# Performance work log

Measured on AMD Instinct MI355X. Metric: run time of the kernel, lower is better.

The kernel has to match this reference:

```python
import jax, jax.numpy as jnp
import numpy as np

B, L, D = 4, 512, 1024
E, TOP_K = 16, 4
F = 4 * D  # expert hidden width


def setup_inputs() -> dict:
    key = jax.random.key(0)
    ks = jax.random.split(key, 6)
    scale = 0.02
    return {
        "x": jax.random.normal(ks[0], (B, L, D), jnp.float32),
        "keys": jax.random.normal(ks[1], (E, D), jnp.float32),          # expert_keys
        "w1": jax.random.normal(ks[2], (E, F, D), jnp.float32) * scale,  # Linear(D,4D).weight per expert
        "b1": jnp.zeros((E, F), jnp.float32),
        "w2": jax.random.normal(ks[3], (E, D, F), jnp.float32) * scale,  # Linear(4D,D).weight per expert
        "b2": jnp.zeros((E, D), jnp.float32),
        "rw": jax.random.normal(ks[4], (E, D), jnp.float32) * scale,     # router Linear(D,E).weight
        "rb": jnp.zeros((E,), jnp.float32),
    }


def reference(x, keys, w1, b1, w2, b2, rw, rb):
    # Laplace gate: squared Euclidean distance token-to-expert-key (broadcasted, as in torch)
    diff = x[:, :, None, :] - keys                      # (B,L,E,D)
    dist2 = jnp.sum(diff * diff, axis=-1)               # (B,L,E)
    logits = -dist2 + jnp.einsum('bld,ed->ble', x, rw) + rb

    topv, topi = jax.lax.top_k(logits, TOP_K)           # (B,L,K)
    w = jax.nn.softmax(topv, axis=-1)                   # (B,L,K)

    # Dense all-expert MLP (exact GELU, matching torch nn.GELU default)
    hidden = jax.nn.gelu(jnp.einsum('bld,efd->blef', x, w1) + b1, approximate=False)  # (B,L,E,F)
    exp_out = jnp.einsum('blef,edf->bled', hidden, w2) + b2                            # (B,L,E,D)

    # Gather top-k expert outputs and combine with softmax weights
    sel = jnp.take_along_axis(exp_out, topi[..., None], axis=2)  # (B,L,K,D)
    fused = jnp.sum(w[..., None] * sel, axis=2)                  # (B,L,D)
    return fused
```

## Files before the change

### kernel.cpp

```cpp
#include <hip/hip_runtime.h>

#define B_ 4
#define L_ 512
#define D_ 1024
#define E_ 16
#define K_ 4
#define F_ 4096
#define NTOK (B_*L_)
#define NPAIR (NTOK*K_)

typedef float f32x4 __attribute__((ext_vector_type(4)));
typedef __bf16 bf16x8 __attribute__((ext_vector_type(8)));

__device__ inline unsigned int pack2(float a, float b) {
    unsigned short ua = __builtin_bit_cast(unsigned short, (__bf16)a);
    unsigned short ub = __builtin_bit_cast(unsigned short, (__bf16)b);
    return (unsigned int)ua | ((unsigned int)ub << 16);
}

__global__ __launch_bounds__(256) void router_kernel(
    const float* __restrict__ x, const float* __restrict__ keys,
    const float* __restrict__ rw, const float* __restrict__ rb,
    int* __restrict__ topi, float* __restrict__ topw, int* __restrict__ counts)
{
    int t = blockIdx.x;
    int tid = threadIdx.x;
    if (blockIdx.x == 0 && tid < E_) counts[tid] = 0;

    __shared__ float xs[D_];
    const float* xrow = x + (size_t)t * D_;
    for (int i = tid; i < D_; i += 256) xs[i] = xrow[i];
    __syncthreads();

    int e    = tid >> 4;
    int lane = tid & 15;
    const float* krow = keys + e * D_;
    const float* rrow = rw   + e * D_;
    double dist2 = 0.0, dot = 0.0;
    for (int d = lane; d < D_; d += 16) {
        float xv = xs[d];
        float df = xv - krow[d];
        dist2 += (double)df * df;
        dot   += (double)xv * rrow[d];
    }
    #pragma unroll
    for (int m = 8; m >= 1; m >>= 1) {
        dist2 += __shfl_xor(dist2, m);
        dot   += __shfl_xor(dot, m);
    }
    __shared__ float lg[E_];
    if (lane == 0) lg[e] = (float)(-dist2 + dot) + rb[e];
    __syncthreads();

    if (tid == 0) {
        float v[E_];
        #pragma unroll
        for (int i = 0; i < E_; i++) v[i] = lg[i];
        int   idx[K_]; float val[K_];
        #pragma unroll
        for (int k = 0; k < K_; k++) {
            int bi = 0; float bv = -1e30f;
            #pragma unroll
            for (int i = 0; i < E_; i++) if (v[i] > bv) { bv = v[i]; bi = i; }
            idx[k] = bi; val[k] = bv; v[bi] = -1e30f;
        }
        float mx = val[0], s = 0.f, w[K_];
        #pragma unroll
        for (int k = 0; k < K_; k++) { w[k] = expf(val[k] - mx); s += w[k]; }
        float inv = 1.0f / s;
        #pragma unroll
        for (int k = 0; k < K_; k++) {
            topi[t*K_ + k] = idx[k];
            topw[t*K_ + k] = w[k] * inv;
        }
    }
}

__global__ void bucket_kernel(const int* __restrict__ topi, const float* __restrict__ topw,
                              int* __restrict__ counts,
                              int* __restrict__ bucket_tok, float* __restrict__ bucket_w)
{
    int i = blockIdx.x * 256 + threadIdx.x;
    if (i >= NPAIR) return;
    int t = i >> 2;
    int e = topi[i];
    int pos = atomicAdd(&counts[e], 1);
    bucket_tok[e * NTOK + pos] = t;
    bucket_w [e * NTOK + pos] = topw[i];
}

__global__ void scan_kernel(const int* __restrict__ counts, int* __restrict__ offsets)
{
    if (threadIdx.x == 0) {
        int s = 0;
        for (int e = 0; e < E_; e++) { offsets[e] = s; s += counts[e]; }
        offsets[E_] = s;
    }
}

__global__ __launch_bounds__(256) void gemm1_kernel(
    const float* __restrict__ x, const float* __restrict__ w1, const float* __restrict__ b1,
    const int* __restrict__ counts, const int* __restrict__ offsets,
    const int* __restrict__ bucket_tok, unsigned short* __restrict__ hidden)
{
    int e  = blockIdx.z;
    int Te = counts[e];
    int row0 = blockIdx.y * 128;
    if (row0 >= Te) return;
    int f0 = blockIdx.x * 128;
    int tid = threadIdx.x;

    __shared__ unsigned short As[128][40];
    __shared__ unsigned short Bs[128][40];
    __shared__ int toks[128];

    if (tid < 128) {
        int r = row0 + tid;
        toks[tid] = bucket_tok[e * NTOK + (r < Te ? r : Te - 1)];
    }
    __syncthreads();

    int lane = tid & 63, wave = tid >> 6;
    int wr = wave >> 1, wc = wave & 1;
    int lr = lane & 15;
    int ko = (lane >> 4) * 8;

    f32x4 acc[4][4];
    #pragma unroll
    for (int m = 0; m < 4; m++)
        #pragma unroll
        for (int n = 0; n < 4; n++) acc[m][n] = (f32x4){0.f, 0.f, 0.f, 0.f};

    int sr = tid >> 1;
    int sc = (tid & 1) * 16;

    for (int k0 = 0; k0 < D_; k0 += 32) {
        {
            const float4* s4 = reinterpret_cast<const float4*>(x + (size_t)toks[sr] * D_ + k0 + sc);
            float4 a0 = s4[0], a1 = s4[1], a2 = s4[2], a3 = s4[3];
            uint4 p0 = { pack2(a0.x,a0.y), pack2(a0.z,a0.w), pack2(a1.x,a1.y), pack2(a1.z,a1.w) };
            uint4 p1 = { pack2(a2.x,a2.y), pack2(a2.z,a2.w), pack2(a3.x,a3.y), pack2(a3.z,a3.w) };
            *reinterpret_cast<uint4*>(&As[sr][sc])     = p0;
            *reinterpret_cast<uint4*>(&As[sr][sc + 8]) = p1;
        }
        {
            const float4* s4 = reinterpret_cast<const float4*>(w1 + ((size_t)e * F_ + f0 + sr) * D_ + k0 + sc);
            float4 a0 = s4[0], a1 = s4[1], a2 = s4[2], a3 = s4[3];
            uint4 p0 = { pack2(a0.x,a0.y), pack2(a0.z,a0.w), pack2(a1.x,a1.y), pack2(a1.z,a1.w) };
            uint4 p1 = { pack2(a2.x,a2.y), pack2(a2.z,a2.w), pack2(a3.x,a3.y), pack2(a3.z,a3.w) };
            *reinterpret_cast<uint4*>(&Bs[sr][sc])     = p0;
            *reinterpret_cast<uint4*>(&Bs[sr][sc + 8]) = p1;
        }
        __syncthreads();
        bf16x8 a[4], b[4];
        #pragma unroll
        for (int m = 0; m < 4; m++) a[m] = *reinterpret_cast<const bf16x8*>(&As[wr*64 + m*16 + lr][ko]);
        #pragma unroll
        for (int n = 0; n < 4; n++) b[n] = *reinterpret_cast<const bf16x8*>(&Bs[wc*64 + n*16 + lr][ko]);
        #pragma unroll
        for (int m = 0; m < 4; m++)
            #pragma unroll
            for (int n = 0; n < 4; n++)
                acc[m][n] = __builtin_amdgcn_mfma_f32_16x16x32_bf16(a[m], b[n], acc[m][n], 0, 0, 0);
        __syncthreads();
    }

    int obase = offsets[e];
    #pragma unroll
    for (int m = 0; m < 4; m++) {
        int rbase = wr*64 + m*16 + (lane >> 4) * 4;
        #pragma unroll
        for (int n = 0; n < 4; n++) {
            int gcol = f0 + wc*64 + n*16 + lr;
            float bias = b1[e * F_ + gcol];
            #pragma unroll
            for (int r = 0; r < 4; r++) {
                int lrow = rbase + r;
                if (row0 + lrow < Te) {
                    float v = acc[m][n][r] + bias;
                    float g = 0.5f * v * (1.0f + erff(v * 0.70710678118654752f));
                    hidden[(size_t)(obase + row0 + lrow) * F_ + gcol] =
                        __builtin_bit_cast(unsigned short, (__bf16)g);
                }
            }
        }
    }
}

__global__ __launch_bounds__(256) void gemm2_kernel(
    const unsigned short* __restrict__ hidden, const float* __restrict__ w2, const float* __restrict__ b2,
    const int* __restrict__ counts, const int* __restrict__ offsets,
    const int* __restrict__ bucket_tok, const float* __restrict__ bucket_w,
    float* __restrict__ out)
{
    int e  = blockIdx.z;
    int Te = counts[e];
    int row0 = blockIdx.y * 128;
    if (row0 >= Te) return;
    int n0 = blockIdx.x * 128;
    int tid = threadIdx.x;

    __shared__ unsigned short As[128][40];
    __shared__ unsigned short Bs[128][40];
    __shared__ int   toks[128];
    __shared__ float wts [128];

    if (tid < 128) {
        int r = row0 + tid;
        int rc = (r < Te ? r : Te - 1);
        toks[tid] = bucket_tok[e * NTOK + rc];
        wts [tid] = bucket_w [e * NTOK + rc];
    }
    __syncthreads();

    int lane = tid & 63, wave = tid >> 6;
    int wr = wave >> 1, wc = wave & 1;
    int lr = lane & 15;
    int ko = (lane >> 4) * 8;

    f32x4 acc[4][4];
    #pragma unroll
    for (int m = 0; m < 4; m++)
        #pragma unroll
        for (int n = 0; n < 4; n++) acc[m][n] = (f32x4){0.f, 0.f, 0.f, 0.f};

    int sr = tid >> 1;
    int sc = (tid & 1) * 16;
    int obase = offsets[e];
    int arow = row0 + sr; arow = (arow < Te ? arow : Te - 1);
    const uint4* asrc_base = reinterpret_cast<const uint4*>(hidden + (size_t)(obase + arow) * F_);

    for (int k0 = 0; k0 < F_; k0 += 32) {
        {
            const uint4* s = reinterpret_cast<const uint4*>(
                reinterpret_cast<const unsigned short*>(asrc_base) + k0 + sc);
            uint4 p0 = s[0], p1 = s[1];
            *reinterpret_cast<uint4*>(&As[sr][sc])     = p0;
            *reinterpret_cast<uint4*>(&As[sr][sc + 8]) = p1;
        }
        {
            const float4* s4 = reinterpret_cast<const float4*>(w2 + ((size_t)e * D_ + n0 + sr) * F_ + k0 + sc);
            float4 a0 = s4[0], a1 = s4[1], a2 = s4[2], a3 = s4[3];
            uint4 p0 = { pack2(a0.x,a0.y), pack2(a0.z,a0.w), pack2(a1.x,a1.y), pack2(a1.z,a1.w) };
            uint4 p1 = { pack2(a2.x,a2.y), pack2(a2.z,a2.w), pack2(a3.x,a3.y), pack2(a3.z,a3.w) };
            *reinterpret_cast<uint4*>(&Bs[sr][sc])     = p0;
            *reinterpret_cast<uint4*>(&Bs[sr][sc + 8]) = p1;
        }
        __syncthreads();
        bf16x8 a[4], b[4];
        #pragma unroll
        for (int m = 0; m < 4; m++) a[m] = *reinterpret_cast<const bf16x8*>(&As[wr*64 + m*16 + lr][ko]);
        #pragma unroll
        for (int n = 0; n < 4; n++) b[n] = *reinterpret_cast<const bf16x8*>(&Bs[wc*64 + n*16 + lr][ko]);
        #pragma unroll
        for (int m = 0; m < 4; m++)
            #pragma unroll
            for (int n = 0; n < 4; n++)
                acc[m][n] = __builtin_amdgcn_mfma_f32_16x16x32_bf16(a[m], b[n], acc[m][n], 0, 0, 0);
        __syncthreads();
    }

    #pragma unroll
    for (int m = 0; m < 4; m++) {
        int rbase = wr*64 + m*16 + (lane >> 4) * 4;
        #pragma unroll
        for (int n = 0; n < 4; n++) {
            int gcol = n0 + wc*64 + n*16 + lr;
            float bias = b2[e * D_ + gcol];
            #pragma unroll
            for (int r = 0; r < 4; r++) {
                int lrow = rbase + r;
                if (row0 + lrow < Te) {
                    float v = acc[m][n][r] + bias;
                    atomicAdd(&out[(size_t)toks[lrow] * D_ + gcol], wts[lrow] * v);
                }
            }
        }
    }
}

extern "C" void kernel_launch(void* const* d_in, const int* in_sizes, int n_in,
                              void* d_out, int out_size, void* d_ws, size_t ws_size,
                              hipStream_t stream)
{
    const float* x    = (const float*)d_in[0];
    const float* keys = (const float*)d_in[1];
    const float* w1   = (const float*)d_in[2];
    const float* b1   = (const float*)d_in[3];
    const float* w2   = (const float*)d_in[4];
    const float* b2   = (const float*)d_in[5];
    const float* rw   = (const float*)d_in[6];
    const float* rb   = (const float*)d_in[7];
    float* out = (float*)d_out;

    char* wsp = (char*)d_ws;
    size_t off = 0;
    auto alloc = [&](size_t bytes) -> char* {
        char* p = wsp + off;
        off = (off + bytes + 255) & ~(size_t)255;
        return p;
    };
    int*   topi       = (int*)  alloc(NPAIR * sizeof(int));
    float* topw       = (float*)alloc(NPAIR * sizeof(float));
    int*   counts     = (int*)  alloc(E_ * sizeof(int));
    int*   offsets    = (int*)  alloc((E_ + 1) * sizeof(int));
    int*   bucket_tok = (int*)  alloc((size_t)E_ * NTOK * sizeof(int));
    float* bucket_w   = (float*)alloc((size_t)E_ * NTOK * sizeof(float));
    unsigned short* hidden = (unsigned short*)alloc((size_t)NPAIR * F_ * sizeof(unsigned short));

    hipMemsetAsync(d_out, 0, (size_t)out_size * sizeof(float), stream);

    router_kernel<<<NTOK, 256, 0, stream>>>(x, keys, rw, rb, topi, topw, counts);
    bucket_kernel<<<NPAIR / 256, 256, 0, stream>>>(topi, topw, counts, bucket_tok, bucket_w);
    scan_kernel<<<1, 64, 0, stream>>>(counts, offsets);
    gemm1_kernel<<<dim3(F_ / 128, NTOK / 128, E_), 256, 0, stream>>>(
        x, w1, b1, counts, offsets, bucket_tok, hidden);
    gemm2_kernel<<<dim3(D_ / 128, NTOK / 128, E_), 256, 0, stream>>>(
        hidden, w2, b2, counts, offsets, bucket_tok, bucket_w, out);
}
```

Measured before the change: 1.070 ms.

## Pre-convert x and expert weights to bf16, stage tiles via global_load_lds

Adds a conversion kernel that writes bf16 copies of x, w1 and w2 to workspace each call. Both grouped GEMMs then load bf16 tiles straight into LDS with the direct global-to-LDS load builtin, removing the per-tile fp32 load, pack and LDS store done in registers. The cost is an extra full read of the fp32 weights (about 512MB) plus a 256MB bf16 write every call. LDS rows lose their padding, which may add bank conflicts on the MFMA fragment reads.

```diff
diff --git a/kernel.cpp b/kernel.cpp
--- a/kernel.cpp
+++ b/kernel.cpp
@@ -16,6 +16,22 @@
     unsigned short ua = __builtin_bit_cast(unsigned short, (__bf16)a);
     unsigned short ub = __builtin_bit_cast(unsigned short, (__bf16)b);
     return (unsigned int)ua | ((unsigned int)ub << 16);
+}
+
+#define GLOAD16(g, l) __builtin_amdgcn_global_load_lds( \
+    (const __attribute__((address_space(1))) void*)(g), \
+    (__attribute__((address_space(3))) void*)(l), 16, 0, 0)
+
+__global__ __launch_bounds__(256) void cvt_kernel(const float* __restrict__ src,
+                                                  unsigned short* __restrict__ dst)
+{
+    size_t i = ((size_t)blockIdx.x * 256 + threadIdx.x) * 16;
+    const float4* s = reinterpret_cast<const float4*>(src + i);
+    float4 v0 = s[0], v1 = s[1], v2 = s[2], v3 = s[3];
+    uint4 p0 = { pack2(v0.x,v0.y), pack2(v0.z,v0.w), pack2(v1.x,v1.y), pack2(v1.z,v1.w) };
+    uint4 p1 = { pack2(v2.x,v2.y), pack2(v2.z,v2.w), pack2(v3.x,v3.y), pack2(v3.z,v3.w) };
+    uint4* d = reinterpret_cast<uint4*>(dst + i);
+    d[0] = p0; d[1] = p1;
 }
 
 __global__ __launch_bounds__(256) void router_kernel(
@@ -99,7 +115,8 @@
 }
 
 __global__ __launch_bounds__(256) void gemm1_kernel(
-    const float* __restrict__ x, const float* __restrict__ w1, const float* __restrict__ b1,
+    const unsigned short* __restrict__ xb, const unsigned short* __restrict__ w1b,
+    const float* __restrict__ b1,
     const int* __restrict__ counts, const int* __restrict__ offsets,
     const int* __restrict__ bucket_tok, unsigned short* __restrict__ hidden)
 {
@@ -109,9 +126,10 @@
     if (row0 >= Te) return;
     int f0 = blockIdx.x * 128;
     int tid = threadIdx.x;
-
-    __shared__ unsigned short As[128][40];
-    __shared__ unsigned short Bs[128][40];
+    int lane = tid & 63, wave = tid >> 6;
+
+    __shared__ unsigned short As[128][32];
+    __shared__ unsigned short Bs[128][32];
     __shared__ int toks[128];
 
     if (tid < 128) {
@@ -120,10 +138,20 @@
     }
     __syncthreads();
 
-    int lane = tid & 63, wave = tid >> 6;
+    int sl = lane & 3;
+    int r0 = (wave * 2 + 0) * 16 + (lane >> 2);
+    int r1 = (wave * 2 + 1) * 16 + (lane >> 2);
+    const unsigned short* pa0 = xb + (size_t)toks[r0] * D_ + sl * 8;
+    const unsigned short* pa1 = xb + (size_t)toks[r1] * D_ + sl * 8;
+    const unsigned short* pb0 = w1b + ((size_t)e * F_ + f0 + r0) * D_ + sl * 8;
+    const unsigned short* pb1 = w1b + ((size_t)e * F_ + f0 + r1) * D_ + sl * 8;
+    unsigned short* la0 = &As[(wave * 2 + 0) * 16][0];
+    unsigned short* la1 = &As[(wave * 2 + 1) * 16][0];
+    unsigned short* lb0 = &Bs[(wave * 2 + 0) * 16][0];
+    unsigned short* lb1 = &Bs[(wave * 2 + 1) * 16][0];
+
     int wr = wave >> 1, wc = wave & 1;
-    int lr = lane & 15;
-    int ko = (lane >> 4) * 8;
+    int lr = lane & 15, ko = (lane >> 4) * 8;
 
     f32x4 acc[4][4];
     #pragma unroll
@@ -131,26 +159,11 @@
         #pragma unroll
         for (int n = 0; n < 4; n++) acc[m][n] = (f32x4){0.f, 0.f, 0.f, 0.f};
 
-    int sr = tid >> 1;
-    int sc = (tid & 1) * 16;
-
     for (int k0 = 0; k0 < D_; k0 += 32) {
-        {
-            const float4* s4 = reinterpret_cast<const float4*>(x + (size_t)toks[sr] * D_ + k0 + sc);
-            float4 a0 = s4[0], a1 = s4[1], a2 = s4[2], a3 = s4[3];
-            uint4 p0 = { pack2(a0.x,a0.y), pack2(a0.z,a0.w), pack2(a1.x,a1.y), pack2(a1.z,a1.w) };
-            uint4 p1 = { pack2(a2.x,a2.y), pack2(a2.z,a2.w), pack2(a3.x,a3.y), pack2(a3.z,a3.w) };
-            *reinterpret_cast<uint4*>(&As[sr][sc])     = p0;
-            *reinterpret_cast<uint4*>(&As[sr][sc + 8]) = p1;
-        }
-        {
-            const float4* s4 = reinterpret_cast<const float4*>(w1 + ((size_t)e * F_ + f0 + sr) * D_ + k0 + sc);
-            float4 a0 = s4[0], a1 = s4[1], a2 = s4[2], a3 = s4[3];
-            uint4 p0 = { pack2(a0.x,a0.y), pack2(a0.z,a0.w), pack2(a1.x,a1.y), pack2(a1.z,a1.w) };
-            uint4 p1 = { pack2(a2.x,a2.y), pack2(a2.z,a2.w), pack2(a3.x,a3.y), pack2(a3.z,a3.w) };
-            *reinterpret_cast<uint4*>(&Bs[sr][sc])     = p0;
-            *reinterpret_cast<uint4*>(&Bs[sr][sc + 8]) = p1;
-        }
+        GLOAD16(pa0 + k0, la0);
+        GLOAD16(pa1 + k0, la1);
+        GLOAD16(pb0 + k0, lb0);
+        GLOAD16(pb1 + k0, lb1);
         __syncthreads();
         bf16x8 a[4], b[4];
         #pragma unroll
@@ -188,7 +201,8 @@
 }
 
 __global__ __launch_bounds__(256) void gemm2_kernel(
-    const unsigned short* __restrict__ hidden, const float* __restrict__ w2, const float* __restrict__ b2,
+    const unsigned short* __restrict__ hidden, const unsigned short* __restrict__ w2b,
+    const float* __restrict__ b2,
     const int* __restrict__ counts, const int* __restrict__ offsets,
     const int* __restrict__ bucket_tok, const float* __restrict__ bucket_w,
     float* __restrict__ out)
@@ -199,12 +213,14 @@
     if (row0 >= Te) return;
     int n0 = blockIdx.x * 128;
     int tid = threadIdx.x;
-
-    __shared__ unsigned short As[128][40];
-    __shared__ unsigned short Bs[128][40];
+    int lane = tid & 63, wave = tid >> 6;
+
+    __shared__ unsigned short As[128][32];
+    __shared__ unsigned short Bs[128][32];
     __shared__ int   toks[128];
     __shared__ float wts [128];
 
+    int obase = offsets[e];
     if (tid < 128) {
         int r = row0 + tid;
         int rc = (r < Te ? r : Te - 1);
@@ -213,10 +229,22 @@
     }
     __syncthreads();
 
-    int lane = tid & 63, wave = tid >> 6;
+    int sl = lane & 3;
+    int r0 = (wave * 2 + 0) * 16 + (lane >> 2);
+    int r1 = (wave * 2 + 1) * 16 + (lane >> 2);
+    int ar0 = row0 + r0; ar0 = (ar0 < Te ? ar0 : Te - 1);
+    int ar1 = row0 + r1; ar1 = (ar1 < Te ? ar1 : Te - 1);
+    const unsigned short* pa0 = hidden + (size_t)(obase + ar0) * F_ + sl * 8;
+    const unsigned short* pa1 = hidden + (size_t)(obase + ar1) * F_ + sl * 8;
+    const unsigned short* pb0 = w2b + ((size_t)e * D_ + n0 + r0) * F_ + sl * 8;
+    const unsigned short* pb1 = w2b + ((size_t)e * D_ + n0 + r1) * F_ + sl * 8;
+    unsigned short* la0 = &As[(wave * 2 + 0) * 16][0];
+    unsigned short* la1 = &As[(wave * 2 + 1) * 16][0];
+    unsigned short* lb0 = &Bs[(wave * 2 + 0) * 16][0];
+    unsigned short* lb1 = &Bs[(wave * 2 + 1) * 16][0];
+
     int wr = wave >> 1, wc = wave & 1;
-    int lr = lane & 15;
-    int ko = (lane >> 4) * 8;
+    int lr = lane & 15, ko = (lane >> 4) * 8;
 
     f32x4 acc[4][4];
     #pragma unroll
@@ -224,28 +252,11 @@
         #pragma unroll
         for (int n = 0; n < 4; n++) acc[m][n] = (f32x4){0.f, 0.f, 0.f, 0.f};
 
-    int sr = tid >> 1;
-    int sc = (tid & 1) * 16;
-    int obase = offsets[e];
-    int arow = row0 + sr; arow = (arow < Te ? arow : Te - 1);
-    const uint4* asrc_base = reinterpret_cast<const uint4*>(hidden + (size_t)(obase + arow) * F_);
-
     for (int k0 = 0; k0 < F_; k0 += 32) {
-        {
-            const uint4* s = reinterpret_cast<const uint4*>(
-                reinterpret_cast<const unsigned short*>(asrc_base) + k0 + sc);
-            uint4 p0 = s[0], p1 = s[1];
-            *reinterpret_cast<uint4*>(&As[sr][sc])     = p0;
-            *reinterpret_cast<uint4*>(&As[sr][sc + 8]) = p1;
-        }
-        {
-            const float4* s4 = reinterpret_cast<const float4*>(w2 + ((size_t)e * D_ + n0 + sr) * F_ + k0 + sc);
-            float4 a0 = s4[0], a1 = s4[1], a2 = s4[2], a3 = s4[3];
-            uint4 p0 = { pack2(a0.x,a0.y), pack2(a0.z,a0.w), pack2(a1.x,a1.y), pack2(a1.z,a1.w) };
-            uint4 p1 = { pack2(a2.x,a2.y), pack2(a2.z,a2.w), pack2(a3.x,a3.y), pack2(a3.z,a3.w) };
-            *reinterpret_cast<uint4*>(&Bs[sr][sc])     = p0;
-            *reinterpret_cast<uint4*>(&Bs[sr][sc + 8]) = p1;
-        }
+        GLOAD16(pa0 + k0, la0);
+        GLOAD16(pa1 + k0, la1);
+        GLOAD16(pb0 + k0, lb0);
+        GLOAD16(pb1 + k0, lb1);
         __syncthreads();
         bf16x8 a[4], b[4];
         #pragma unroll
@@ -306,6 +317,9 @@
     int*   offsets    = (int*)  alloc((E_ + 1) * sizeof(int));
     int*   bucket_tok = (int*)  alloc((size_t)E_ * NTOK * sizeof(int));
     float* bucket_w   = (float*)alloc((size_t)E_ * NTOK * sizeof(float));
+    unsigned short* xb     = (unsigned short*)alloc((size_t)NTOK * D_ * sizeof(unsigned short));
+    unsigned short* w1b    = (unsigned short*)alloc((size_t)E_ * F_ * D_ * sizeof(unsigned short));
+    unsigned short* w2b    = (unsigned short*)alloc((size_t)E_ * D_ * F_ * sizeof(unsigned short));
     unsigned short* hidden = (unsigned short*)alloc((size_t)NPAIR * F_ * sizeof(unsigned short));
 
     hipMemsetAsync(d_out, 0, (size_t)out_size * sizeof(float), stream);
@@ -313,8 +327,13 @@
     router_kernel<<<NTOK, 256, 0, stream>>>(x, keys, rw, rb, topi, topw, counts);
     bucket_kernel<<<NPAIR / 256, 256, 0, stream>>>(topi, topw, counts, bucket_tok, bucket_w);
     scan_kernel<<<1, 64, 0, stream>>>(counts, offsets);
+
+    cvt_kernel<<<(NTOK * D_) / 4096, 256, 0, stream>>>(x, xb);
+    cvt_kernel<<<(E_ * F_ * D_) / 4096, 256, 0, stream>>>(w1, w1b);
+    cvt_kernel<<<(E_ * D_ * F_) / 4096, 256, 0, stream>>>(w2, w2b);
+
     gemm1_kernel<<<dim3(F_ / 128, NTOK / 128, E_), 256, 0, stream>>>(
-        x, w1, b1, counts, offsets, bucket_tok, hidden);
+        xb, w1b, b1, counts, offsets, bucket_tok, hidden);
     gemm2_kernel<<<dim3(D_ / 128, NTOK / 128, E_), 256, 0, stream>>>(
-        hidden, w2, b2, counts, offsets, bucket_tok, bucket_w, out);
-}
+        hidden, w2b, b2, counts, offsets, bucket_tok, bucket_w, out);
+}
```

Result: faster. 993.5 us (-7.1%).
